# Performance work log

Measured on AMD Instinct MI355X. Metric: run time of the kernel, lower is better.

Reference implementation:

```python
import jax, jax.numpy as jnp
import numpy as np

H = 2048        # hidden_size
NH = 16         # num attention heads
NKV = 4         # num kv heads
HD = H // NH    # head_dim = 128
I = 1024        # expert intermediate size
E = 16          # num experts
TOPK = 2
T = 2048        # num tokens
EPS = 1e-5
THETA = 10000.0


def setup_inputs() -> dict:
    key = jax.random.key(0)
    ks = jax.random.split(key, 12)
    s = 0.02
    return {
        "hidden_states": jax.random.normal(ks[0], (T, H), jnp.float32),
        "ln_in_w": jnp.ones((H,), jnp.float32),
        "ln_post_w": jnp.ones((H,), jnp.float32),
        "ln_res_w": jnp.ones((H,), jnp.float32),
        "wqkv": s * jax.random.normal(ks[1], (H, NH * HD + 2 * NKV * HD), jnp.float32),
        "wo": s * jax.random.normal(ks[2], (NH * HD, H), jnp.float32),
        "res_w13": s * jax.random.normal(ks[3], (H, 2 * H), jnp.float32),
        "res_w2": s * jax.random.normal(ks[4], (H, H), jnp.float32),
        "gate_w": s * jax.random.normal(ks[5], (H, E), jnp.float32),
        "ws": s * jax.random.normal(ks[6], (E, 2 * I, H), jnp.float32),
        "w2s": s * jax.random.normal(ks[7], (E, H, I), jnp.float32),
        "positions": jnp.arange(T, dtype=jnp.int64),
    }


def rms_norm(x, w):
    var = jnp.mean(x * x, axis=-1, keepdims=True)
    return x * jax.lax.rsqrt(var + EPS) * w


def rope_neox(x, positions):
    # x: [T, nheads, HD]; neox style: rotate first/second halves
    half = HD // 2
    inv_freq = 1.0 / (THETA ** (jnp.arange(0, HD, 2, dtype=jnp.float32) / HD))
    ang = positions.astype(jnp.float32)[:, None] * inv_freq  # [T, half]
    cos = jnp.cos(ang)[:, None, :]  # [T,1,half]
    sin = jnp.sin(ang)[:, None, :]
    x1, x2 = x[..., :half], x[..., half:]
    return jnp.concatenate([x1 * cos - x2 * sin, x2 * cos + x1 * sin], axis=-1)


def attention(x, positions, wqkv, wo):
    qkv = x @ wqkv
    q, k, v = jnp.split(qkv, [NH * HD, NH * HD + NKV * HD], axis=-1)
    q = q.reshape(T, NH, HD)
    k = k.reshape(T, NKV, HD)
    v = v.reshape(T, NKV, HD)
    q = rope_neox(q, positions)
    k = rope_neox(k, positions)
    # GQA: repeat kv heads
    rep = NH // NKV
    k = jnp.repeat(k, rep, axis=1)  # [T, NH, HD]
    v = jnp.repeat(v, rep, axis=1)
    scale = HD ** -0.5
    scores = jnp.einsum('thd,shd->hts', q, k) * scale  # [NH, T, T]
    causal = positions[:, None] >= positions[None, :]
    scores = jnp.where(causal[None, :, :], scores, -jnp.inf)
    probs = jax.nn.softmax(scores, axis=-1)
    out = jnp.einsum('hts,shd->thd', probs, v).reshape(T, NH * HD)
    return out @ wo


def silu_and_mul(gu):
    g, u = jnp.split(gu, 2, axis=-1)
    return jax.nn.silu(g) * u


def moe(x, gate_w, ws, w2s):
    logits = x @ gate_w                      # [T, E]
    probs = jax.nn.softmax(logits, axis=-1)
    topw, topi = jax.lax.top_k(probs, TOPK)  # [T, k]
    topw = topw / jnp.sum(topw, axis=-1, keepdims=True)  # renormalize (top_k>1)
    out = jnp.zeros_like(x)
    for e in range(E):
        w_te = jnp.sum(jnp.where(topi == e, topw, 0.0), axis=-1)  # [T]
        gu = x @ ws[e].T                     # [T, 2I]
        h = silu_and_mul(gu)                 # [T, I]
        out = out + w_te[:, None] * (h @ w2s[e].T)
    return out


def reference(hidden_states, ln_in_w, ln_post_w, ln_res_w, wqkv, wo,
              res_w13, res_w2, gate_w, ws, w2s, positions):
    residual_input = hidden_states
    h = rms_norm(hidden_states, ln_in_w)
    h = attention(h, positions, wqkv, wo)
    h = residual_input + h
    residual_attn = h
    # residual MLP branch (use_residual=True)
    h2 = rms_norm(h, ln_res_w)
    h2 = silu_and_mul(h2 @ res_w13) @ res_w2
    residual_mlp = h2
    # NOTE: post_attention_layernorm is applied to residual_input (pre-attn input)
    h3 = rms_norm(residual_input, ln_post_w)
    h3 = moe(h3, gate_w, ws, w2s)
    h = residual_mlp + h3
    return residual_attn + h
```

## Files before the change

### kernel.cpp

```cpp
#include <hip/hip_runtime.h>
#include <math.h>

#define T_    2048
#define H_    2048
#define NH_   16
#define NKV_  4
#define HD_   128
#define I_    1024
#define E_    16
#define QKVN  3072
#define EPS_  1e-5f

typedef __attribute__((ext_vector_type(8))) __bf16 bf16x8;
typedef __attribute__((ext_vector_type(4))) __bf16 bf16x4;
typedef __attribute__((ext_vector_type(4))) float f32x4;
typedef __attribute__((ext_vector_type(8))) unsigned short ushort8v;
typedef __attribute__((ext_vector_type(4))) unsigned short ushort4v;

__device__ __forceinline__ unsigned short f2bf(float f) {
  union { float f; unsigned u; } v; v.f = f;
  return (unsigned short)((v.u + 0x7fffu + ((v.u >> 16) & 1u)) >> 16);
}
__device__ __forceinline__ float bf2f(unsigned short h) {
  union { unsigned u; float f; } v; v.u = ((unsigned)h) << 16;
  return v.f;
}
__device__ __forceinline__ void ldsdma16(const void* g, void* l) {
  __builtin_amdgcn_global_load_lds((const __attribute__((address_space(1))) void*)g,
                                   (__attribute__((address_space(3))) void*)l, 16, 0, 0);
}

__global__ __launch_bounds__(256) void rmsnorm_bf_k(const float* __restrict__ x,
                                                    const float* __restrict__ w,
                                                    unsigned short* __restrict__ out) {
  int t = blockIdx.x;
  const float* xr = x + (size_t)t * H_;
  float ss = 0.f;
  for (int c = threadIdx.x; c < H_; c += 256) { float v = xr[c]; ss += v * v; }
#pragma unroll
  for (int off = 32; off > 0; off >>= 1) ss += __shfl_xor(ss, off);
  __shared__ float wsum[4];
  __shared__ float srstd;
  int wid = threadIdx.x >> 6;
  if ((threadIdx.x & 63) == 0) wsum[wid] = ss;
  __syncthreads();
  if (threadIdx.x == 0) {
    float tot = wsum[0] + wsum[1] + wsum[2] + wsum[3];
    srstd = rsqrtf(tot * (1.f / H_) + EPS_);
  }
  __syncthreads();
  float r = srstd;
  unsigned short* orow = out + (size_t)t * H_;
  for (int c = threadIdx.x; c < H_; c += 256) orow[c] = f2bf(xr[c] * r * w[c]);
}

__global__ __launch_bounds__(256) void transp_bf_k(const float* __restrict__ in,
                                                   unsigned short* __restrict__ out,
                                                   int K, int N) {
  __shared__ float tile[32][33];
  int k0 = blockIdx.y * 32, n0 = blockIdx.x * 32;
  int c = threadIdx.x & 31, r = threadIdx.x >> 5;
  for (int rr = r; rr < 32; rr += 8)
    tile[rr][c] = in[(size_t)(k0 + rr) * N + n0 + c];
  __syncthreads();
  for (int rr = r; rr < 32; rr += 8)
    out[(size_t)(n0 + rr) * K + k0 + c] = f2bf(tile[c][rr]);
}

#define BM 128
#define BN 128
#define BK 32
__global__ __launch_bounds__(256) void gemm_mfma_tn(const unsigned short* __restrict__ A,
                                                    const unsigned short* __restrict__ Bt,
                                                    float* __restrict__ C,
                                                    int M, int N, int K) {
  __shared__ unsigned short sA[BM * BK];
  __shared__ unsigned short sB[BN * BK];
  const int tid = threadIdx.x;
  const int wave = tid >> 6;
  const int lane = tid & 63;
  const int m0 = blockIdx.y * BM;
  const int n0 = blockIdx.x * BN;
  const int wm = (wave & 1) * 64;
  const int wn = (wave >> 1) * 64;
  const int srow = wave * 32 + (lane >> 2);
  const int sch  = (lane & 3) * 8;
  const unsigned short* ga0 = A  + (size_t)(m0 + srow) * K + sch;
  const unsigned short* ga1 = A  + (size_t)(m0 + srow + 16) * K + sch;
  const unsigned short* gb0 = Bt + (size_t)(n0 + srow) * K + sch;
  const unsigned short* gb1 = Bt + (size_t)(n0 + srow + 16) * K + sch;
  unsigned short* la0 = &sA[(wave * 32) * BK];
  unsigned short* la1 = &sA[(wave * 32 + 16) * BK];
  unsigned short* lb0 = &sB[(wave * 32) * BK];
  unsigned short* lb1 = &sB[(wave * 32 + 16) * BK];
  const int frm = lane & 15;
  const int quad = lane >> 4;
  f32x4 acc[4][4] = {};
  for (int k0 = 0; k0 < K; k0 += BK) {
    ldsdma16(ga0, la0);
    ldsdma16(ga1, la1);
    ldsdma16(gb0, lb0);
    ldsdma16(gb1, lb1);
    ga0 += BK; ga1 += BK; gb0 += BK; gb1 += BK;
    __syncthreads();
    bf16x8 af[4], bf[4];
#pragma unroll
    for (int i = 0; i < 4; ++i) {
      af[i] = *(const bf16x8*)&sA[(wm + i * 16 + frm) * BK + quad * 8];
      bf[i] = *(const bf16x8*)&sB[(wn + i * 16 + frm) * BK + quad * 8];
    }
#pragma unroll
    for (int i = 0; i < 4; ++i)
#pragma unroll
      for (int j = 0; j < 4; ++j)
        acc[i][j] = __builtin_amdgcn_mfma_f32_16x16x32_bf16(af[i], bf[j], acc[i][j], 0, 0, 0);
    __syncthreads();
  }
#pragma unroll
  for (int i = 0; i < 4; ++i) {
    int rbase = m0 + wm + i * 16 + quad * 4;
#pragma unroll
    for (int j = 0; j < 4; ++j) {
      int c = n0 + wn + j * 16 + frm;
      float* cp = C + (size_t)rbase * N + c;
#pragma unroll
      for (int r = 0; r < 4; ++r) cp[(size_t)r * N] = acc[i][j][r];
    }
  }
}

__global__ __launch_bounds__(256) void gemm_mfma_routed(const unsigned short* __restrict__ A, int lda,
                                                        const float* __restrict__ B,
                                                        float* __restrict__ C, int ldc,
                                                        const int* __restrict__ gather,
                                                        const int* __restrict__ offsets,
                                                        int N, int K) {
  const int e = blockIdx.z;
  const int rs = offsets[e], re = offsets[e + 1];
  const int r0 = rs + blockIdx.y * BM;
  if (r0 >= re) return;
  const int n0 = blockIdx.x * BN;
  const float* Be = B + (size_t)e * N * K;
  __shared__ unsigned short sA[BM * BK];
  __shared__ unsigned short sB[BN * BK];
  const int tid = threadIdx.x;
  const int wave = tid >> 6;
  const int lane = tid & 63;
  const int wm = (wave & 1) * 64;
  const int wn = (wave >> 1) * 64;
  int ra0 = r0 + wave * 32 + (lane >> 2);
  int ra1 = ra0 + 16;
  int c0 = ra0 < re ? ra0 : re - 1;
  int c1 = ra1 < re ? ra1 : re - 1;
  int src0 = gather ? gather[c0] : c0;
  int src1 = gather ? gather[c1] : c1;
  const int sch = (lane & 3) * 8;
  const unsigned short* ga0 = A + (size_t)src0 * lda + sch;
  const unsigned short* ga1 = A + (size_t)src1 * lda + sch;
  unsigned short* la0 = &sA[(wave * 32) * BK];
  unsigned short* la1 = &sA[(wave * 32 + 16) * BK];
  const int brow = tid >> 1;
  const int bk = (tid & 1) * 16;
  const float* bp0 = Be + (size_t)(n0 + brow) * K + bk;
  unsigned short* bdst = &sB[brow * BK + bk];
  const int frm = lane & 15;
  const int quad = lane >> 4;
  f32x4 acc[4][4] = {};
  for (int k0 = 0; k0 < K; k0 += BK) {
    ldsdma16(ga0, la0);
    ldsdma16(ga1, la1);
    ga0 += BK; ga1 += BK;
    const float* bp = bp0 + k0;
#pragma unroll
    for (int q = 0; q < 4; ++q) {
      float4 v = *(const float4*)(bp + q * 4);
      bdst[q * 4 + 0] = f2bf(v.x);
      bdst[q * 4 + 1] = f2bf(v.y);
      bdst[q * 4 + 2] = f2bf(v.z);
      bdst[q * 4 + 3] = f2bf(v.w);
    }
    __syncthreads();
    bf16x8 af[4], bfr[4];
#pragma unroll
    for (int i = 0; i < 4; ++i) {
      af[i]  = *(const bf16x8*)&sA[(wm + i * 16 + frm) * BK + quad * 8];
      bfr[i] = *(const bf16x8*)&sB[(wn + i * 16 + frm) * BK + quad * 8];
    }
#pragma unroll
    for (int i = 0; i < 4; ++i)
#pragma unroll
      for (int j = 0; j < 4; ++j)
        acc[i][j] = __builtin_amdgcn_mfma_f32_16x16x32_bf16(af[i], bfr[j], acc[i][j], 0, 0, 0);
    __syncthreads();
  }
#pragma unroll
  for (int i = 0; i < 4; ++i) {
    int rbase = r0 + wm + i * 16 + quad * 4;
#pragma unroll
    for (int j = 0; j < 4; ++j) {
      int c = n0 + wn + j * 16 + frm;
#pragma unroll
      for (int r = 0; r < 4; ++r) {
        int rr = rbase + r;
        if (rr < re) C[(size_t)rr * ldc + c] = acc[i][j][r];
      }
    }
  }
}

__global__ __launch_bounds__(256) void rope_k(float* __restrict__ qkv) {
  int idx = blockIdx.x * 256 + threadIdx.x;
  const int total = T_ * (NH_ + NKV_) * 64;
  if (idx >= total) return;
  int i = idx & 63;
  int head = (idx >> 6) % (NH_ + NKV_);
  int t = idx / (64 * (NH_ + NKV_));
  float* base = qkv + (size_t)t * QKVN + (head < NH_ ? head * HD_ : NH_ * HD_ + (head - NH_) * HD_);
  float inv = powf(10000.f, -(float)i * (1.f / 64.f));
  float ang = (float)t * inv;
  float c = cosf(ang), s = sinf(ang);
  float x1 = base[i], x2 = base[i + 64];
  base[i]      = x1 * c - x2 * s;
  base[i + 64] = x2 * c + x1 * s;
}

__global__ __launch_bounds__(256) void flash_attn_mfma_k(const float* __restrict__ qkv,
                                                         unsigned short* __restrict__ out) {
  const int h   = blockIdx.x;
  const int qt  = (T_ / 64 - 1) - blockIdx.y;
  const int kvh = h >> 2;
  const int tid = threadIdx.x;
  const int wave = tid >> 6, lane = tid & 63;
  const int frm = lane & 15, quad = lane >> 4;
  const int q0w = qt * 64 + wave * 16;

  __shared__ unsigned short sK[32 * 128];
  __shared__ unsigned short sVt[128 * 32];
  __shared__ unsigned short sP[4][16 * 36];

  const float scale = 0.08838834764831845f;

  bf16x8 qf[4];
  {
    const float* qrow = qkv + (size_t)(q0w + frm) * QKVN + h * HD_;
#pragma unroll
    for (int ks = 0; ks < 4; ++ks) {
      float4 u = *(const float4*)(qrow + ks * 32 + quad * 8);
      float4 v = *(const float4*)(qrow + ks * 32 + quad * 8 + 4);
      union { ushort8v u; bf16x8 b; } cv;
      cv.u[0] = f2bf(u.x); cv.u[1] = f2bf(u.y); cv.u[2] = f2bf(u.z); cv.u[3] = f2bf(u.w);
      cv.u[4] = f2bf(v.x); cv.u[5] = f2bf(v.y); cv.u[6] = f2bf(v.z); cv.u[7] = f2bf(v.w);
      qf[ks] = cv.b;
    }
  }

  float m[4] = {-INFINITY, -INFINITY, -INFINITY, -INFINITY};
  float l[4] = {0.f, 0.f, 0.f, 0.f};
  f32x4 oacc[8] = {};

  const int srow = tid >> 3;
  const int sc8  = tid & 7;
  const int nt   = 2 * qt + 2;

  for (int kt = 0; kt < nt; ++kt) {
    const int s0 = kt * 32;
    {
      const float* krow = qkv + (size_t)(s0 + srow) * QKVN + NH_ * HD_ + kvh * HD_;
      const float* vrow = krow + NKV_ * HD_;
#pragma unroll
      for (int c = 0; c < 4; ++c) {
        const int d0 = sc8 * 4 + c * 32;
        float4 kv4 = *(const float4*)(krow + d0);
        float4 vv4 = *(const float4*)(vrow + d0);
        ushort4v kw;
        kw[0] = f2bf(kv4.x); kw[1] = f2bf(kv4.y); kw[2] = f2bf(kv4.z); kw[3] = f2bf(kv4.w);
        unsigned koff = ((unsigned)(srow * 256 + d0 * 2)) ^ ((unsigned)(srow & 7) << 4);
        *(ushort4v*)((char*)sK + koff) = kw;
        float vv[4] = {vv4.x, vv4.y, vv4.z, vv4.w};
#pragma unroll
        for (int j = 0; j < 4; ++j) {
          const unsigned d = d0 + j;
          unsigned voff = (d * 64u + (unsigned)srow * 2u) ^ (((d >> 2) & 3u) << 4);
          *(unsigned short*)((char*)sVt + voff) = f2bf(vv[j]);
        }
      }
    }
    __syncthreads();

    if (s0 <= q0w + 15) {
      f32x4 sacc[2] = {};
#pragma unroll
      for (int sub = 0; sub < 2; ++sub) {
        const int row = sub * 16 + frm;
        const unsigned swz = (unsigned)(row & 7) << 4;
#pragma unroll
        for (int ks = 0; ks < 4; ++ks) {
          unsigned koff = ((unsigned)(row * 256 + (ks * 32 + quad * 8) * 2)) ^ swz;
          bf16x8 kf = *(const bf16x8*)((char*)sK + koff);
          sacc[sub] = __builtin_amdgcn_mfma_f32_16x16x32_bf16(qf[ks], kf, sacc[sub], 0, 0, 0);
        }
      }
      const bool edge = (s0 + 31 > q0w);
      unsigned short* sPw = sP[wave];
#pragma unroll
      for (int r = 0; r < 4; ++r) {
        float s0v = sacc[0][r] * scale;
        float s1v = sacc[1][r] * scale;
        const int qi = q0w + quad * 4 + r;
        if (edge) {
          if (s0 + frm > qi)      s0v = -INFINITY;
          if (s0 + 16 + frm > qi) s1v = -INFINITY;
        }
        float mx = fmaxf(s0v, s1v);
        mx = fmaxf(mx, __shfl_xor(mx, 1));
        mx = fmaxf(mx, __shfl_xor(mx, 2));
        mx = fmaxf(mx, __shfl_xor(mx, 4));
        mx = fmaxf(mx, __shfl_xor(mx, 8));
        const float mnew = fmaxf(m[r], mx);
        const float p0 = __expf(s0v - mnew);
        const float p1 = __expf(s1v - mnew);
        float rs = p0 + p1;
        rs += __shfl_xor(rs, 1);
        rs += __shfl_xor(rs, 2);
        rs += __shfl_xor(rs, 4);
        rs += __shfl_xor(rs, 8);
        const float alpha = __expf(m[r] - mnew);
        l[r] = l[r] * alpha + rs;
        m[r] = mnew;
        sPw[(quad * 4 + r) * 36 + frm]      = f2bf(p0);
        sPw[(quad * 4 + r) * 36 + frm + 16] = f2bf(p1);
#pragma unroll
        for (int dt = 0; dt < 8; ++dt) oacc[dt][r] *= alpha;
      }
      bf16x4 plo = *(const bf16x4*)&sPw[frm * 36 + quad * 8];
      bf16x4 phi = *(const bf16x4*)&sPw[frm * 36 + quad * 8 + 4];
      bf16x8 pa = __builtin_shufflevector(plo, phi, 0, 1, 2, 3, 4, 5, 6, 7);
#pragma unroll
      for (int dt = 0; dt < 8; ++dt) {
        const unsigned drow = dt * 16 + frm;
        unsigned voff = (drow * 64u + (unsigned)quad * 16u) ^ (((drow >> 2) & 3u) << 4);
        bf16x8 vf = *(const bf16x8*)((char*)sVt + voff);
        oacc[dt] = __builtin_amdgcn_mfma_f32_16x16x32_bf16(pa, vf, oacc[dt], 0, 0, 0);
      }
    }
    __syncthreads();
  }

#pragma unroll
  for (int r = 0; r < 4; ++r) {
    const float linv = 1.f / l[r];
    const int row = q0w + quad * 4 + r;
    unsigned short* orow = out + (size_t)row * (NH_ * HD_) + h * HD_;
#pragma unroll
    for (int dt = 0; dt < 8; ++dt)
      orow[dt * 16 + frm] = f2bf(oacc[dt][r] * linv);
  }
}

__global__ __launch_bounds__(256) void add_k(const float* __restrict__ a, float* __restrict__ b, int n) {
  int idx = blockIdx.x * 256 + threadIdx.x;
  if (idx < n) b[idx] = a[idx] + b[idx];
}

__global__ __launch_bounds__(256) void silu_mul_bf_k(const float* __restrict__ in,
                                                     unsigned short* __restrict__ out,
                                                     int rows, int n) {
  int idx = blockIdx.x * 256 + threadIdx.x;
  if (idx >= rows * n) return;
  int r = idx / n, c = idx - r * n;
  float g = in[(size_t)r * 2 * n + c];
  float u = in[(size_t)r * 2 * n + n + c];
  out[(size_t)r * n + c] = f2bf((g / (1.f + expf(-g))) * u);
}

__global__ __launch_bounds__(256) void gate_fp32_k(const float* __restrict__ hidden,
                                                   const float* __restrict__ lnw,
                                                   const float* __restrict__ gw,
                                                   float* __restrict__ logits) {
  int t = blockIdx.x;
  const float* xr = hidden + (size_t)t * H_;
  float ss = 0.f;
  for (int c = threadIdx.x; c < H_; c += 256) { float v = xr[c]; ss += v * v; }
#pragma unroll
  for (int off = 32; off > 0; off >>= 1) ss += __shfl_xor(ss, off);
  __shared__ float wsum[4];
  __shared__ float srstd;
  int wid = threadIdx.x >> 6;
  if ((threadIdx.x & 63) == 0) wsum[wid] = ss;
  __syncthreads();
  if (threadIdx.x == 0) {
    float tot = wsum[0] + wsum[1] + wsum[2] + wsum[3];
    srstd = rsqrtf(tot * (1.f / H_) + EPS_);
  }
  __syncthreads();
  float r = srstd;
  int e = threadIdx.x & 15;
  int chunk = threadIdx.x >> 4;
  float s = 0.f;
  for (int c = chunk * 128; c < chunk * 128 + 128; ++c)
    s += xr[c] * r * lnw[c] * gw[c * E_ + e];
  __shared__ float red[16][16];
  red[chunk][e] = s;
  __syncthreads();
  if (threadIdx.x < 16) {
    float tot = 0.f;
    for (int c2 = 0; c2 < 16; ++c2) tot += red[c2][threadIdx.x];
    logits[(size_t)t * E_ + threadIdx.x] = tot;
  }
}

__global__ __launch_bounds__(256) void gate_topk_k(const float* __restrict__ logits,
                                                   int* __restrict__ counts,
                                                   int* __restrict__ topi,
                                                   float* __restrict__ topw) {
  int t = blockIdx.x * 256 + threadIdx.x;
  if (t >= T_) return;
  float l[E_];
  float mx = -INFINITY;
  for (int e = 0; e < E_; ++e) { l[e] = logits[t * E_ + e]; mx = fmaxf(mx, l[e]); }
  for (int e = 0; e < E_; ++e) l[e] = expf(l[e] - mx);
  int i0 = 0;
  for (int e = 1; e < E_; ++e) if (l[e] > l[i0]) i0 = e;
  int i1 = (i0 == 0) ? 1 : 0;
  for (int e = 0; e < E_; ++e) if (e != i0 && l[e] > l[i1]) i1 = e;
  float p0 = l[i0], p1 = l[i1];
  float inv = 1.f / (p0 + p1);
  topi[t * 2] = i0; topi[t * 2 + 1] = i1;
  topw[t * 2] = p0 * inv; topw[t * 2 + 1] = p1 * inv;
  atomicAdd(&counts[i0], 1);
  atomicAdd(&counts[i1], 1);
}

__global__ void make_offsets_k(const int* __restrict__ counts, int* __restrict__ offsets,
                               int* __restrict__ fill) {
  if (threadIdx.x == 0 && blockIdx.x == 0) {
    int acc = 0;
    for (int e = 0; e < E_; ++e) { offsets[e] = acc; fill[e] = acc; acc += counts[e]; }
    offsets[E_] = acc;
  }
}

__global__ __launch_bounds__(256) void scatter_k(const int* __restrict__ topi,
                                                 int* __restrict__ fill,
                                                 int* __restrict__ routed_token,
                                                 int* __restrict__ token_rows) {
  int t = blockIdx.x * 256 + threadIdx.x;
  if (t >= T_) return;
  for (int k = 0; k < 2; ++k) {
    int e = topi[t * 2 + k];
    int row = atomicAdd(&fill[e], 1);
    routed_token[row] = t;
    token_rows[t * 2 + k] = row;
  }
}

__global__ __launch_bounds__(256) void final_k(const float* __restrict__ resid_attn,
                                               const float* __restrict__ res_mlp,
                                               const float* __restrict__ moe_rows,
                                               const int* __restrict__ token_rows,
                                               const float* __restrict__ topw,
                                               float* __restrict__ out) {
  int idx = blockIdx.x * 256 + threadIdx.x;
  if (idx >= T_ * H_) return;
  int t = idx >> 11, c = idx & (H_ - 1);
  int r0 = token_rows[t * 2], r1 = token_rows[t * 2 + 1];
  float w0 = topw[t * 2], w1 = topw[t * 2 + 1];
  out[idx] = resid_attn[idx] + res_mlp[idx]
           + w0 * moe_rows[(size_t)r0 * H_ + c]
           + w1 * moe_rows[(size_t)r1 * H_ + c];
}

extern "C" void kernel_launch(void* const* d_in, const int* in_sizes, int n_in,
                              void* d_out, int out_size, void* d_ws, size_t ws_size,
                              hipStream_t stream) {
  const float* hidden    = (const float*)d_in[0];
  const float* ln_in_w   = (const float*)d_in[1];
  const float* ln_post_w = (const float*)d_in[2];
  const float* ln_res_w  = (const float*)d_in[3];
  const float* wqkv      = (const float*)d_in[4];
  const float* wo        = (const float*)d_in[5];
  const float* res_w13   = (const float*)d_in[6];
  const float* res_w2    = (const float*)d_in[7];
  const float* gate_w    = (const float*)d_in[8];
  const float* ws_moe    = (const float*)d_in[9];
  const float* w2s       = (const float*)d_in[10];
  float* out = (float*)d_out;

  const size_t TH = (size_t)T_ * H_;
  char* p = (char*)d_ws;
  auto alloc = [&](size_t bytes) { char* q = p; p += (bytes + 255) & ~(size_t)255; return q; };
  unsigned short* wqkv_t = (unsigned short*)alloc((size_t)QKVN * H_ * 2);
  unsigned short* wo_t   = (unsigned short*)alloc((size_t)H_ * H_ * 2);
  unsigned short* w13_t  = (unsigned short*)alloc((size_t)4096 * H_ * 2);
  unsigned short* w2_t   = (unsigned short*)alloc((size_t)H_ * H_ * 2);
  float* qkv      = (float*)alloc((size_t)T_ * QKVN * 4);
  float* gu       = (float*)alloc((size_t)T_ * 4096 * 4);
  float* moe_rows = (float*)alloc((size_t)4096 * H_ * 4);
  float* resid    = (float*)alloc(TH * 4);
  unsigned short* bfA          = (unsigned short*)alloc(TH * 2);
  unsigned short* x_ln_post_bf = (unsigned short*)alloc(TH * 2);
  unsigned short* attn_bf      = (unsigned short*)alloc(TH * 2);
  float* logits = (float*)alloc((size_t)T_ * E_ * 4);
  float* topw   = (float*)alloc((size_t)T_ * 2 * 4);
  int* counts       = (int*)alloc(16 * 4);
  int* offsets      = (int*)alloc(24 * 4);
  int* fill         = (int*)alloc(16 * 4);
  int* topi         = (int*)alloc((size_t)T_ * 2 * 4);
  int* token_rows   = (int*)alloc((size_t)T_ * 2 * 4);
  int* routed_token = (int*)alloc((size_t)T_ * 2 * 4);
  float* res_mlp = qkv;
  float* moe_gu  = gu;

  transp_bf_k<<<dim3(QKVN / 32, H_ / 32), 256, 0, stream>>>(wqkv, wqkv_t, H_, QKVN);
  transp_bf_k<<<dim3(H_ / 32, H_ / 32), 256, 0, stream>>>(wo, wo_t, H_, H_);
  transp_bf_k<<<dim3(4096 / 32, H_ / 32), 256, 0, stream>>>(res_w13, w13_t, H_, 4096);
  transp_bf_k<<<dim3(H_ / 32, H_ / 32), 256, 0, stream>>>(res_w2, w2_t, H_, H_);
  rmsnorm_bf_k<<<T_, 256, 0, stream>>>(hidden, ln_in_w, bfA);
  rmsnorm_bf_k<<<T_, 256, 0, stream>>>(hidden, ln_post_w, x_ln_post_bf);
  gemm_mfma_tn<<<dim3(QKVN / BN, T_ / BM), 256, 0, stream>>>(bfA, wqkv_t, qkv, T_, QKVN, H_);
  rope_k<<<(T_ * (NH_ + NKV_) * 64 + 255) / 256, 256, 0, stream>>>(qkv);
  flash_attn_mfma_k<<<dim3(NH_, T_ / 64), 256, 0, stream>>>(qkv, attn_bf);
  gemm_mfma_tn<<<dim3(H_ / BN, T_ / BM), 256, 0, stream>>>(attn_bf, wo_t, resid, T_, H_, H_);
  add_k<<<(int)(TH / 256), 256, 0, stream>>>(hidden, resid, (int)TH);
  rmsnorm_bf_k<<<T_, 256, 0, stream>>>(resid, ln_res_w, attn_bf);
  gemm_mfma_tn<<<dim3(4096 / BN, T_ / BM), 256, 0, stream>>>(attn_bf, w13_t, gu, T_, 4096, H_);
  silu_mul_bf_k<<<(int)(TH / 256), 256, 0, stream>>>(gu, bfA, T_, H_);
  gemm_mfma_tn<<<dim3(H_ / BN, T_ / BM), 256, 0, stream>>>(bfA, w2_t, res_mlp, T_, H_, H_);
  gate_fp32_k<<<T_, 256, 0, stream>>>(hidden, ln_post_w, gate_w, logits);
  hipMemsetAsync(counts, 0, 16 * sizeof(int), stream);
  gate_topk_k<<<T_ / 256, 256, 0, stream>>>(logits, counts, topi, topw);
  make_offsets_k<<<1, 64, 0, stream>>>(counts, offsets, fill);
  scatter_k<<<T_ / 256, 256, 0, stream>>>(topi, fill, routed_token, token_rows);
  gemm_mfma_routed<<<dim3(2 * I_ / BN, 4096 / BM, E_), 256, 0, stream>>>(
      x_ln_post_bf, H_, ws_moe, moe_gu, 2 * I_, routed_token, offsets, 2 * I_, H_);
  silu_mul_bf_k<<<(int)(TH / 256), 256, 0, stream>>>(moe_gu, bfA, 2 * T_, I_);
  gemm_mfma_routed<<<dim3(H_ / BN, 4096 / BM, E_), 256, 0, stream>>>(
      bfA, I_, w2s, moe_rows, H_, nullptr, offsets, H_, I_);
  final_k<<<(int)(TH / 256), 256, 0, stream>>>(resid, res_mlp, moe_rows, token_rows, topw, out);
}
```

Before: 1.166 ms.

## Split-K dense GEMMs with atomics and split-KV flash attention with combine

```diff
diff --git a/kernel.cpp b/kernel.cpp
--- a/kernel.cpp
+++ b/kernel.cpp
@@ -81,14 +81,17 @@
   const int lane = tid & 63;
   const int m0 = blockIdx.y * BM;
   const int n0 = blockIdx.x * BN;
+  const int nz = gridDim.z;
+  const int kper = K / nz;
+  const int kbeg = blockIdx.z * kper;
   const int wm = (wave & 1) * 64;
   const int wn = (wave >> 1) * 64;
   const int srow = wave * 32 + (lane >> 2);
   const int sch  = (lane & 3) * 8;
-  const unsigned short* ga0 = A  + (size_t)(m0 + srow) * K + sch;
-  const unsigned short* ga1 = A  + (size_t)(m0 + srow + 16) * K + sch;
-  const unsigned short* gb0 = Bt + (size_t)(n0 + srow) * K + sch;
-  const unsigned short* gb1 = Bt + (size_t)(n0 + srow + 16) * K + sch;
+  const unsigned short* ga0 = A  + (size_t)(m0 + srow) * K + kbeg + sch;
+  const unsigned short* ga1 = A  + (size_t)(m0 + srow + 16) * K + kbeg + sch;
+  const unsigned short* gb0 = Bt + (size_t)(n0 + srow) * K + kbeg + sch;
+  const unsigned short* gb1 = Bt + (size_t)(n0 + srow + 16) * K + kbeg + sch;
   unsigned short* la0 = &sA[(wave * 32) * BK];
   unsigned short* la1 = &sA[(wave * 32 + 16) * BK];
   unsigned short* lb0 = &sB[(wave * 32) * BK];
@@ -96,7 +99,7 @@
   const int frm = lane & 15;
   const int quad = lane >> 4;
   f32x4 acc[4][4] = {};
-  for (int k0 = 0; k0 < K; k0 += BK) {
+  for (int k0 = 0; k0 < kper; k0 += BK) {
     ldsdma16(ga0, la0);
     ldsdma16(ga1, la1);
     ldsdma16(gb0, lb0);
@@ -116,6 +119,7 @@
         acc[i][j] = __builtin_amdgcn_mfma_f32_16x16x32_bf16(af[i], bf[j], acc[i][j], 0, 0, 0);
     __syncthreads();
   }
+  const bool single = (nz == 1);
 #pragma unroll
   for (int i = 0; i < 4; ++i) {
     int rbase = m0 + wm + i * 16 + quad * 4;
@@ -124,7 +128,10 @@
       int c = n0 + wn + j * 16 + frm;
       float* cp = C + (size_t)rbase * N + c;
 #pragma unroll
-      for (int r = 0; r < 4; ++r) cp[(size_t)r * N] = acc[i][j][r];
+      for (int r = 0; r < 4; ++r) {
+        if (single) cp[(size_t)r * N] = acc[i][j][r];
+        else        atomicAdd(&cp[(size_t)r * N], acc[i][j][r]);
+      }
     }
   }
 }
@@ -224,19 +231,24 @@
   base[i + 64] = x2 * c + x1 * s;
 }
 
-__global__ __launch_bounds__(256) void flash_attn_mfma_k(const float* __restrict__ qkv,
-                                                         unsigned short* __restrict__ out) {
-  const int h   = blockIdx.x;
-  const int qt  = (T_ / 64 - 1) - blockIdx.y;
+__global__ __launch_bounds__(256) void flash_attn_splitk_k(const float* __restrict__ qkv,
+                                                           float* __restrict__ partO,
+                                                           float* __restrict__ partML) {
+  const int h = blockIdx.x;
+  const int y = blockIdx.y;
+  int qt, ch;
+  if (y < 17)      { qt = 15 + y;        ch = 0; }
+  else if (y < 33) { qt = 31 - (y - 17); ch = 1; }
+  else             { qt = 14 - (y - 33); ch = 0; }
   const int kvh = h >> 2;
   const int tid = threadIdx.x;
   const int wave = tid >> 6, lane = tid & 63;
   const int frm = lane & 15, quad = lane >> 4;
   const int q0w = qt * 64 + wave * 16;
 
-  __shared__ unsigned short sK[32 * 128];
-  __shared__ unsigned short sVt[128 * 32];
-  __shared__ unsigned short sP[4][16 * 36];
+  __shared__ unsigned short sK[64 * 128];
+  __shared__ unsigned short sVt[128 * 64];
+  __shared__ unsigned short sP[4][16 * 72];
 
   const float scale = 0.08838834764831845f;
 
@@ -258,68 +270,73 @@
   float l[4] = {0.f, 0.f, 0.f, 0.f};
   f32x4 oacc[8] = {};
 
-  const int srow = tid >> 3;
-  const int sc8  = tid & 7;
-  const int nt   = 2 * qt + 2;
-
-  for (int kt = 0; kt < nt; ++kt) {
-    const int s0 = kt * 32;
-    {
-      const float* krow = qkv + (size_t)(s0 + srow) * QKVN + NH_ * HD_ + kvh * HD_;
-      const float* vrow = krow + NKV_ * HD_;
-#pragma unroll
-      for (int c = 0; c < 4; ++c) {
-        const int d0 = sc8 * 4 + c * 32;
-        float4 kv4 = *(const float4*)(krow + d0);
-        float4 vv4 = *(const float4*)(vrow + d0);
+  const int sthr = tid & 127;
+  const bool doV = tid >= 128;
+  const int kt0 = ch * 16;
+  const int ktend = (qt < kt0 + 15) ? qt : (kt0 + 15);
+
+  for (int kt = kt0; kt <= ktend; ++kt) {
+    const int s0 = kt * 64;
+    if (doV) {
+      const int d = sthr;
+      const float* vcol = qkv + (size_t)s0 * QKVN + (NH_ + NKV_) * HD_ + kvh * HD_ + d;
+#pragma unroll
+      for (int c = 0; c < 8; ++c) {
+        ushort8v pk;
+#pragma unroll
+        for (int j = 0; j < 8; ++j) pk[j] = f2bf(vcol[(size_t)(c * 8 + j) * QKVN]);
+        unsigned off = ((unsigned)(d * 128 + c * 16)) ^ (((unsigned)d & 7u) << 4);
+        *(ushort8v*)((char*)sVt + off) = pk;
+      }
+    } else {
+      const int row = sthr >> 1, half = (sthr & 1) * 64;
+      const float* krow = qkv + (size_t)(s0 + row) * QKVN + NH_ * HD_ + kvh * HD_ + half;
+#pragma unroll
+      for (int c = 0; c < 16; ++c) {
+        float4 k4 = *(const float4*)(krow + c * 4);
         ushort4v kw;
-        kw[0] = f2bf(kv4.x); kw[1] = f2bf(kv4.y); kw[2] = f2bf(kv4.z); kw[3] = f2bf(kv4.w);
-        unsigned koff = ((unsigned)(srow * 256 + d0 * 2)) ^ ((unsigned)(srow & 7) << 4);
-        *(ushort4v*)((char*)sK + koff) = kw;
-        float vv[4] = {vv4.x, vv4.y, vv4.z, vv4.w};
-#pragma unroll
-        for (int j = 0; j < 4; ++j) {
-          const unsigned d = d0 + j;
-          unsigned voff = (d * 64u + (unsigned)srow * 2u) ^ (((d >> 2) & 3u) << 4);
-          *(unsigned short*)((char*)sVt + voff) = f2bf(vv[j]);
-        }
+        kw[0] = f2bf(k4.x); kw[1] = f2bf(k4.y); kw[2] = f2bf(k4.z); kw[3] = f2bf(k4.w);
+        unsigned off = ((unsigned)(row * 256 + half * 2 + c * 8)) ^ (((unsigned)row & 7u) << 4);
+        *(ushort4v*)((char*)sK + off) = kw;
       }
     }
     __syncthreads();
 
-    if (s0 <= q0w + 15) {
-      f32x4 sacc[2] = {};
-#pragma unroll
-      for (int sub = 0; sub < 2; ++sub) {
+    if (s0 <= q0w) {
+      f32x4 sacc[4] = {};
+#pragma unroll
+      for (int sub = 0; sub < 4; ++sub) {
         const int row = sub * 16 + frm;
-        const unsigned swz = (unsigned)(row & 7) << 4;
+        const unsigned swz = ((unsigned)row & 7u) << 4;
 #pragma unroll
         for (int ks = 0; ks < 4; ++ks) {
-          unsigned koff = ((unsigned)(row * 256 + (ks * 32 + quad * 8) * 2)) ^ swz;
+          unsigned koff = ((unsigned)(row * 256 + ks * 64 + quad * 16)) ^ swz;
           bf16x8 kf = *(const bf16x8*)((char*)sK + koff);
           sacc[sub] = __builtin_amdgcn_mfma_f32_16x16x32_bf16(qf[ks], kf, sacc[sub], 0, 0, 0);
         }
       }
-      const bool edge = (s0 + 31 > q0w);
+      const bool edge = (s0 + 63 > q0w);
       unsigned short* sPw = sP[wave];
 #pragma unroll
       for (int r = 0; r < 4; ++r) {
-        float s0v = sacc[0][r] * scale;
-        float s1v = sacc[1][r] * scale;
+        float sv[4];
+#pragma unroll
+        for (int sub = 0; sub < 4; ++sub) sv[sub] = sacc[sub][r] * scale;
         const int qi = q0w + quad * 4 + r;
         if (edge) {
-          if (s0 + frm > qi)      s0v = -INFINITY;
-          if (s0 + 16 + frm > qi) s1v = -INFINITY;
+#pragma unroll
+          for (int sub = 0; sub < 4; ++sub)
+            if (s0 + sub * 16 + frm > qi) sv[sub] = -INFINITY;
         }
-        float mx = fmaxf(s0v, s1v);
+        float mx = fmaxf(fmaxf(sv[0], sv[1]), fmaxf(sv[2], sv[3]));
         mx = fmaxf(mx, __shfl_xor(mx, 1));
         mx = fmaxf(mx, __shfl_xor(mx, 2));
         mx = fmaxf(mx, __shfl_xor(mx, 4));
         mx = fmaxf(mx, __shfl_xor(mx, 8));
         const float mnew = fmaxf(m[r], mx);
-        const float p0 = __expf(s0v - mnew);
-        const float p1 = __expf(s1v - mnew);
-        float rs = p0 + p1;
+        float p[4], rs = 0.f;
+#pragma unroll
+        for (int sub = 0; sub < 4; ++sub) { p[sub] = __expf(sv[sub] - mnew); rs += p[sub]; }
         rs += __shfl_xor(rs, 1);
         rs += __shfl_xor(rs, 2);
         rs += __shfl_xor(rs, 4);
@@ -327,34 +344,68 @@
         const float alpha = __expf(m[r] - mnew);
         l[r] = l[r] * alpha + rs;
         m[r] = mnew;
-        sPw[(quad * 4 + r) * 36 + frm]      = f2bf(p0);
-        sPw[(quad * 4 + r) * 36 + frm + 16] = f2bf(p1);
+#pragma unroll
+        for (int sub = 0; sub < 4; ++sub)
+          sPw[(quad * 4 + r) * 72 + sub * 16 + frm] = f2bf(p[sub]);
 #pragma unroll
         for (int dt = 0; dt < 8; ++dt) oacc[dt][r] *= alpha;
       }
-      bf16x4 plo = *(const bf16x4*)&sPw[frm * 36 + quad * 8];
-      bf16x4 phi = *(const bf16x4*)&sPw[frm * 36 + quad * 8 + 4];
-      bf16x8 pa = __builtin_shufflevector(plo, phi, 0, 1, 2, 3, 4, 5, 6, 7);
+      bf16x8 pa[2];
+#pragma unroll
+      for (int ks = 0; ks < 2; ++ks)
+        pa[ks] = *(const bf16x8*)&sPw[frm * 72 + ks * 32 + quad * 8];
 #pragma unroll
       for (int dt = 0; dt < 8; ++dt) {
-        const unsigned drow = dt * 16 + frm;
-        unsigned voff = (drow * 64u + (unsigned)quad * 16u) ^ (((drow >> 2) & 3u) << 4);
-        bf16x8 vf = *(const bf16x8*)((char*)sVt + voff);
-        oacc[dt] = __builtin_amdgcn_mfma_f32_16x16x32_bf16(pa, vf, oacc[dt], 0, 0, 0);
+        const int drow = dt * 16 + frm;
+        const unsigned swz = ((unsigned)drow & 7u) << 4;
+#pragma unroll
+        for (int ks = 0; ks < 2; ++ks) {
+          unsigned voff = ((unsigned)(drow * 128 + ks * 64 + quad * 16)) ^ swz;
+          bf16x8 vf = *(const bf16x8*)((char*)sVt + voff);
+          oacc[dt] = __builtin_amdgcn_mfma_f32_16x16x32_bf16(pa[ks], vf, oacc[dt], 0, 0, 0);
+        }
       }
     }
     __syncthreads();
   }
 
+  const int plane = h * 2 + ch;
 #pragma unroll
   for (int r = 0; r < 4; ++r) {
-    const float linv = 1.f / l[r];
     const int row = q0w + quad * 4 + r;
-    unsigned short* orow = out + (size_t)row * (NH_ * HD_) + h * HD_;
-#pragma unroll
-    for (int dt = 0; dt < 8; ++dt)
-      orow[dt * 16 + frm] = f2bf(oacc[dt][r] * linv);
-  }
+    float* po = partO + ((size_t)plane * T_ + row) * HD_;
+#pragma unroll
+    for (int dt = 0; dt < 8; ++dt) po[dt * 16 + frm] = oacc[dt][r];
+    if (frm == 0) {
+      float* pml = partML + ((size_t)plane * T_ + row) * 2;
+      pml[0] = m[r]; pml[1] = l[r];
+    }
+  }
+}
+
+__global__ __launch_bounds__(256) void attn_combine_k(const float* __restrict__ partO,
+                                                      const float* __restrict__ partML,
+                                                      unsigned short* __restrict__ out) {
+  int idx = blockIdx.x * 256 + threadIdx.x;
+  const int d = idx & (HD_ - 1);
+  const int row = (idx >> 7) & (T_ - 1);
+  const int h = idx >> 18;
+  const int p0 = h * 2;
+  float m0 = partML[((size_t)p0 * T_ + row) * 2 + 0];
+  float l0 = partML[((size_t)p0 * T_ + row) * 2 + 1];
+  float o0 = partO[((size_t)p0 * T_ + row) * HD_ + d];
+  float val;
+  if (row < 1024) {
+    val = o0 / l0;
+  } else {
+    float m1 = partML[((size_t)(p0 + 1) * T_ + row) * 2 + 0];
+    float l1 = partML[((size_t)(p0 + 1) * T_ + row) * 2 + 1];
+    float o1 = partO[((size_t)(p0 + 1) * T_ + row) * HD_ + d];
+    float M = fmaxf(m0, m1);
+    float w0 = __expf(m0 - M), w1 = __expf(m1 - M);
+    val = (o0 * w0 + o1 * w1) / (l0 * w0 + l1 * w1);
+  }
+  out[(size_t)row * (NH_ * HD_) + h * HD_ + d] = f2bf(val);
 }
 
 __global__ __launch_bounds__(256) void add_k(const float* __restrict__ a, float* __restrict__ b, int n) {
@@ -510,6 +561,8 @@
   int* routed_token = (int*)alloc((size_t)T_ * 2 * 4);
   float* res_mlp = qkv;
   float* moe_gu  = gu;
+  float* partO   = gu;
+  float* partML  = moe_rows;
 
   transp_bf_k<<<dim3(QKVN / 32, H_ / 32), 256, 0, stream>>>(wqkv, wqkv_t, H_, QKVN);
   transp_bf_k<<<dim3(H_ / 32, H_ / 32), 256, 0, stream>>>(wo, wo_t, H_, H_);
@@ -517,15 +570,20 @@
   transp_bf_k<<<dim3(H_ / 32, H_ / 32), 256, 0, stream>>>(res_w2, w2_t, H_, H_);
   rmsnorm_bf_k<<<T_, 256, 0, stream>>>(hidden, ln_in_w, bfA);
   rmsnorm_bf_k<<<T_, 256, 0, stream>>>(hidden, ln_post_w, x_ln_post_bf);
-  gemm_mfma_tn<<<dim3(QKVN / BN, T_ / BM), 256, 0, stream>>>(bfA, wqkv_t, qkv, T_, QKVN, H_);
+  hipMemsetAsync(qkv, 0, (size_t)T_ * QKVN * 4, stream);
+  gemm_mfma_tn<<<dim3(QKVN / BN, T_ / BM, 2), 256, 0, stream>>>(bfA, wqkv_t, qkv, T_, QKVN, H_);
   rope_k<<<(T_ * (NH_ + NKV_) * 64 + 255) / 256, 256, 0, stream>>>(qkv);
-  flash_attn_mfma_k<<<dim3(NH_, T_ / 64), 256, 0, stream>>>(qkv, attn_bf);
-  gemm_mfma_tn<<<dim3(H_ / BN, T_ / BM), 256, 0, stream>>>(attn_bf, wo_t, resid, T_, H_, H_);
+  flash_attn_splitk_k<<<dim3(NH_, 48), 256, 0, stream>>>(qkv, partO, partML);
+  attn_combine_k<<<(NH_ * T_ * HD_) / 256, 256, 0, stream>>>(partO, partML, attn_bf);
+  hipMemsetAsync(resid, 0, TH * 4, stream);
+  gemm_mfma_tn<<<dim3(H_ / BN, T_ / BM, 2), 256, 0, stream>>>(attn_bf, wo_t, resid, T_, H_, H_);
   add_k<<<(int)(TH / 256), 256, 0, stream>>>(hidden, resid, (int)TH);
   rmsnorm_bf_k<<<T_, 256, 0, stream>>>(resid, ln_res_w, attn_bf);
-  gemm_mfma_tn<<<dim3(4096 / BN, T_ / BM), 256, 0, stream>>>(attn_bf, w13_t, gu, T_, 4096, H_);
+  hipMemsetAsync(gu, 0, (size_t)T_ * 4096 * 4, stream);
+  gemm_mfma_tn<<<dim3(4096 / BN, T_ / BM, 2), 256, 0, stream>>>(attn_bf, w13_t, gu, T_, 4096, H_);
   silu_mul_bf_k<<<(int)(TH / 256), 256, 0, stream>>>(gu, bfA, T_, H_);
-  gemm_mfma_tn<<<dim3(H_ / BN, T_ / BM), 256, 0, stream>>>(bfA, w2_t, res_mlp, T_, H_, H_);
+  hipMemsetAsync(res_mlp, 0, TH * 4, stream);
+  gemm_mfma_tn<<<dim3(H_ / BN, T_ / BM, 2), 256, 0, stream>>>(bfA, w2_t, res_mlp, T_, H_, H_);
   gate_fp32_k<<<T_, 256, 0, stream>>>(hidden, ln_post_w, gate_w, logits);
   hipMemsetAsync(counts, 0, 16 * sizeof(int), stream);
   gate_topk_k<<<T_ / 256, 256, 0, stream>>>(logits, counts, topi, topw);
```

Measured after the change: 1.162 ms. Within noise of the previous version (-0.3%).
